# Kernel tuning notes

Hardware: AMD Instinct MI355X
Metric: run time of the kernel (lower is better)

Reference implementation:

```python
import jax, jax.numpy as jnp
import numpy as np


def setup_inputs() -> dict:
    key = jax.random.key(0)
    ks = jax.random.split(key, 5)
    B, Lq, Lk, KD, E, VD = 2, 1024, 1024, 128, 128, 128
    return {
        "query": jax.random.normal(ks[0], (B, Lq, KD), dtype=jnp.float32),
        "key": jax.random.normal(ks[1], (B, Lk, KD), dtype=jnp.float32),
        "value": jax.random.normal(ks[2], (B, Lk, VD), dtype=jnp.float32),
        "vT": jax.random.normal(ks[3], (E,), dtype=jnp.float32) * (1.0 / np.sqrt(E)),
        "weight": jax.random.normal(ks[4], (E, 2 * KD), dtype=jnp.float32) * (1.0 / np.sqrt(2 * KD)),
    }


def reference(query, key, value, vT, weight):
    # Additive (Bahdanau) attention: score(i,j) = vT . tanh(W @ concat(q_i, k_j))
    kdim = query.shape[-1]
    Wq = weight[:, :kdim]   # [E, kdim] acts on query half of concat
    Wk = weight[:, kdim:]   # [E, kdim] acts on key half
    qp = jnp.einsum("bqd,ed->bqe", query, Wq)   # [B, Lq, E]
    kp = jnp.einsum("bkd,ed->bke", key, Wk)     # [B, Lk, E]
    # broadcast-add replaces the explicit concat+linear: [B, Lq, Lk, E]
    h = jnp.tanh(qp[:, :, None, :] + kp[:, None, :, :])
    scores = jnp.einsum("bqke,e->bqk", h, vT)    # [B, Lq, Lk]
    attn = jax.nn.softmax(scores, axis=-1)
    return jnp.einsum("bqk,bkv->bqv", attn, value)  # [B, Lq, Vd]
```

## Files before the change

kernel.cpp:

```cpp
#include <hip/hip_runtime.h>

#define CSC 2.88539008177792681f

typedef float v2f __attribute__((ext_vector_type(2)));

__device__ __forceinline__ float fast_exp2(float x) {
  return __builtin_amdgcn_exp2f(x);
}
__device__ __forceinline__ float fast_rcp(float x) {
  return __builtin_amdgcn_rcpf(x);
}
__device__ __forceinline__ v2f vfma(v2f a, v2f b, v2f c) {
  return __builtin_elementwise_fma(a, b, c);
}
__device__ __forceinline__ v2f vsplat(float s) {
  v2f r;
  r[0] = s;
  r[1] = s;
  return r;
}

__global__ __launch_bounds__(256) void proj_kernel(
    const float* __restrict__ query, const float* __restrict__ key,
    const float* __restrict__ weight, float* __restrict__ Eq,
    float* __restrict__ EkT4) {
  __shared__ __align__(16) float rows[16][128];
  __shared__ __align__(16) float tile[16][132];
  int blk = blockIdx.x;
  bool isK = blk >= 128;
  const float* src = isK ? key : query;
  int woff = isK ? 128 : 0;
  int row0 = (isK ? blk - 128 : blk) * 16;
  int tid = threadIdx.x;
#pragma unroll
  for (int i = 0; i < 8; ++i) {
    int f = i * 256 + tid;
    rows[f >> 7][f & 127] = src[(size_t)row0 * 128 + f];
  }
  __syncthreads();
  int e = tid & 127;
  int rh = (tid >> 7) * 8;
  float acc[8];
#pragma unroll
  for (int i = 0; i < 8; ++i) acc[i] = 0.f;
  const float4* wrow =
      reinterpret_cast<const float4*>(weight + (size_t)e * 256 + woff);
#pragma unroll 4
  for (int d4 = 0; d4 < 32; ++d4) {
    float4 wv = wrow[d4];
#pragma unroll
    for (int i = 0; i < 8; ++i) {
      float4 rv = *reinterpret_cast<const float4*>(&rows[rh + i][d4 * 4]);
      acc[i] = fmaf(rv.x, wv.x, acc[i]);
      acc[i] = fmaf(rv.y, wv.y, acc[i]);
      acc[i] = fmaf(rv.z, wv.z, acc[i]);
      acc[i] = fmaf(rv.w, wv.w, acc[i]);
    }
  }
  if (!isK) {
#pragma unroll
    for (int i = 0; i < 8; ++i)
      Eq[(size_t)(row0 + rh + i) * 128 + e] = fast_exp2(CSC * acc[i]);
  } else {
#pragma unroll
    for (int i = 0; i < 8; ++i) tile[rh + i][e] = fast_exp2(CSC * acc[i]);
    __syncthreads();
    int kk = tid & 15;
    int e4a = tid >> 4;
#pragma unroll
    for (int h = 0; h < 2; ++h) {
      int ee = e4a + h * 16;
      float4 v = *reinterpret_cast<const float4*>(&tile[kk][ee * 4]);
      *reinterpret_cast<float4*>(EkT4 + ((size_t)ee * 2048 + row0 + kk) * 4) =
          v;
    }
  }
}

__global__ __launch_bounds__(512, 4) void attn_kernel(
    const float* __restrict__ Eq, const float* __restrict__ EkT4,
    const float* __restrict__ vT, const float* __restrict__ value,
    float* __restrict__ pblk, float* __restrict__ dsum) {
  __shared__ __align__(16) float sc[8][512];
  __shared__ __align__(16) v2f pout[8][8][64];
  __shared__ float wsum[8][8];

  int tid = threadIdx.x;
  int lane = tid & 63;
  int w = tid >> 6;
  int bi = blockIdx.x;
  int kh = bi & 1;
  int qg = (bi >> 1) & 127;
  int b = bi >> 8;
  int q0 = qg * 8;
  int k0 = kh * 512;

  {
    const float4* ekp = reinterpret_cast<const float4*>(EkT4) +
                        (size_t)b * 1024 + k0 + tid;
    const float* eqb = Eq + (size_t)(b * 1024 + q0) * 128;
    const float4* vtp = reinterpret_cast<const float4*>(vT);
    float acc[8];
#pragma unroll
    for (int q = 0; q < 8; ++q) acc[q] = 0.f;
#pragma unroll 2
    for (int e4 = 0; e4 < 32; ++e4) {
      float4 ek = ekp[(size_t)e4 * 2048];
      float4 vt4 = vtp[e4];
#pragma unroll
      for (int q = 0; q < 8; ++q) {
        float4 eqq = *reinterpret_cast<const float4*>(
            eqb + (size_t)q * 128 + e4 * 4);
        float A0 = fmaf(eqq.x, ek.x, 1.f);
        float A1 = fmaf(eqq.y, ek.y, 1.f);
        float A2 = fmaf(eqq.z, ek.z, 1.f);
        float A3 = fmaf(eqq.w, ek.w, 1.f);
        float P01 = A0 * A1;
        float P23 = A2 * A3;
        float t01 = fmaf(vt4.x, A1, vt4.y * A0);
        float t23 = fmaf(vt4.z, A3, vt4.w * A2);
        float num = fmaf(t23, P01, t01 * P23);
        acc[q] = fmaf(num, fast_rcp(P01 * P23), acc[q]);
      }
    }
#pragma unroll
    for (int q = 0; q < 8; ++q) {
      float p = fast_exp2(-CSC * acc[q]);
      sc[q][tid] = p;
      float s = p;
#pragma unroll
      for (int off = 32; off; off >>= 1) s += __shfl_xor(s, off);
      if (lane == 0) wsum[w][q] = s;
    }
  }
  __syncthreads();
  if (tid < 8) {
    float s = 0.f;
#pragma unroll
    for (int ww = 0; ww < 8; ++ww) s += wsum[ww][tid];
    dsum[(size_t)bi * 8 + tid] = s;
  }

  {
    int kb = w * 64;
    v2f acc2[8];
#pragma unroll
    for (int q = 0; q < 8; ++q) acc2[q] = vsplat(0.f);
    const v2f* vp = reinterpret_cast<const v2f*>(value) +
                    ((size_t)b * 1024 + k0 + kb) * 64 + lane;
#pragma unroll 2
    for (int k4 = 0; k4 < 16; ++k4) {
      v2f vv0 = vp[(size_t)(k4 * 4 + 0) * 64];
      v2f vv1 = vp[(size_t)(k4 * 4 + 1) * 64];
      v2f vv2 = vp[(size_t)(k4 * 4 + 2) * 64];
      v2f vv3 = vp[(size_t)(k4 * 4 + 3) * 64];
#pragma unroll
      for (int q = 0; q < 8; ++q) {
        float4 pp = *reinterpret_cast<const float4*>(&sc[q][kb + k4 * 4]);
        acc2[q] = vfma(vsplat(pp.x), vv0, acc2[q]);
        acc2[q] = vfma(vsplat(pp.y), vv1, acc2[q]);
        acc2[q] = vfma(vsplat(pp.z), vv2, acc2[q]);
        acc2[q] = vfma(vsplat(pp.w), vv3, acc2[q]);
      }
    }
#pragma unroll
    for (int q = 0; q < 8; ++q) pout[w][q][lane] = acc2[q];
  }
  __syncthreads();

  {
    int q = tid >> 6;
    int c = tid & 63;
    v2f r = pout[0][q][c];
#pragma unroll
    for (int ww = 1; ww < 8; ++ww) r = r + pout[ww][q][c];
    *reinterpret_cast<v2f*>(pblk + (size_t)bi * 1024 + q * 128 + 2 * c) = r;
  }
}

__global__ __launch_bounds__(512) void combine_kernel(
    const float* __restrict__ pblk, const float* __restrict__ dsum,
    float* __restrict__ out) {
  int g = blockIdx.x * 512 + threadIdx.x;
  int row = g >> 6;
  int c = g & 63;
  int b = row >> 10;
  int qg = (row >> 3) & 127;
  int q = row & 7;
  int bi0 = b * 256 + qg * 2;
  v2f r0 = *reinterpret_cast<const v2f*>(pblk + (size_t)bi0 * 1024 + q * 128 +
                                         2 * c);
  v2f r1 = *reinterpret_cast<const v2f*>(pblk + (size_t)(bi0 + 1) * 1024 +
                                         q * 128 + 2 * c);
  float d = dsum[(size_t)bi0 * 8 + q] + dsum[(size_t)(bi0 + 1) * 8 + q];
  v2f r = r0 + r1;
  float inv = fast_rcp(d);
  r[0] *= inv;
  r[1] *= inv;
  *reinterpret_cast<v2f*>(out + (size_t)row * 128 + 2 * c) = r;
}

extern "C" void kernel_launch(void* const* d_in, const int* in_sizes, int n_in,
                              void* d_out, int out_size, void* d_ws,
                              size_t ws_size, hipStream_t stream) {
  const float* query = (const float*)d_in[0];
  const float* key = (const float*)d_in[1];
  const float* value = (const float*)d_in[2];
  const float* vT = (const float*)d_in[3];
  const float* weight = (const float*)d_in[4];
  float* out = (float*)d_out;
  float* Eq = (float*)d_ws;
  float* EkT4 = Eq + 262144;
  float* pblk = EkT4 + 262144;
  float* dsum = pblk + 524288;
  proj_kernel<<<256, 256, 0, stream>>>(query, key, weight, Eq, EkT4);
  attn_kernel<<<512, 512, 0, stream>>>(Eq, EkT4, vT, value, pblk, dsum);
  combine_kernel<<<256, 512, 0, stream>>>(pblk, dsum, out);
}
```

Baseline: 48.55 us.

## Split attention keys into four chunks and stage Eq/vT in LDS

The attention kernel now splits each query group's keys into four 256-key chunks, handled by 256-thread blocks, instead of two 512-key chunks, doubling the grid to 1024 blocks. The per-block query exponentials and vT are loaded once into shared memory rather than re-read from global memory inside the inner loop. The combine kernel now sums four partial outputs and denominators, and the workspace layout grows to hold the larger partial buffer. This adds more blocks and more parallel work across CUs at the cost of extra partial-result traffic and a heavier combine step.

```diff
diff --git a/kernel.cpp b/kernel.cpp
--- a/kernel.cpp
+++ b/kernel.cpp
@@ -77,40 +77,51 @@
   }
 }
 
-__global__ __launch_bounds__(512, 4) void attn_kernel(
+__global__ __launch_bounds__(256, 4) void attn_kernel(
     const float* __restrict__ Eq, const float* __restrict__ EkT4,
     const float* __restrict__ vT, const float* __restrict__ value,
     float* __restrict__ pblk, float* __restrict__ dsum) {
-  __shared__ __align__(16) float sc[8][512];
-  __shared__ __align__(16) v2f pout[8][8][64];
-  __shared__ float wsum[8][8];
+  __shared__ __align__(16) float eq_lds[8][128];
+  __shared__ __align__(16) float vt_lds[128];
+  __shared__ __align__(16) float sc[8][256];
+  __shared__ __align__(16) v2f pout[4][8][64];
+  __shared__ float wsum[4][8];
 
   int tid = threadIdx.x;
   int lane = tid & 63;
   int w = tid >> 6;
   int bi = blockIdx.x;
-  int kh = bi & 1;
-  int qg = (bi >> 1) & 127;
-  int b = bi >> 8;
+  int kh = bi & 3;
+  int qg = (bi >> 2) & 127;
+  int b = bi >> 9;
   int q0 = qg * 8;
-  int k0 = kh * 512;
+  int k0 = kh * 256;
 
   {
-    const float4* ekp = reinterpret_cast<const float4*>(EkT4) +
-                        (size_t)b * 1024 + k0 + tid;
-    const float* eqb = Eq + (size_t)(b * 1024 + q0) * 128;
-    const float4* vtp = reinterpret_cast<const float4*>(vT);
+    const float4* eqg =
+        reinterpret_cast<const float4*>(Eq + (size_t)(b * 1024 + q0) * 128);
+    *reinterpret_cast<float4*>(&eq_lds[tid >> 5][(tid & 31) * 4]) = eqg[tid];
+    if (tid < 32)
+      *reinterpret_cast<float4*>(&vt_lds[tid * 4]) =
+          reinterpret_cast<const float4*>(vT)[tid];
+  }
+  __syncthreads();
+
+  {
+    const float4* ekp =
+        reinterpret_cast<const float4*>(EkT4) + (size_t)b * 1024 + k0 + tid;
     float acc[8];
 #pragma unroll
     for (int q = 0; q < 8; ++q) acc[q] = 0.f;
 #pragma unroll 2
     for (int e4 = 0; e4 < 32; ++e4) {
       float4 ek = ekp[(size_t)e4 * 2048];
-      float4 vt4 = vtp[e4];
+      float4 vt4 =
+          *reinterpret_cast<const float4*>(&vt_lds[e4 * 4]);
 #pragma unroll
       for (int q = 0; q < 8; ++q) {
-        float4 eqq = *reinterpret_cast<const float4*>(
-            eqb + (size_t)q * 128 + e4 * 4);
+        float4 eqq =
+            *reinterpret_cast<const float4*>(&eq_lds[q][e4 * 4]);
         float A0 = fmaf(eqq.x, ek.x, 1.f);
         float A1 = fmaf(eqq.y, ek.y, 1.f);
         float A2 = fmaf(eqq.z, ek.z, 1.f);
@@ -135,9 +146,7 @@
   }
   __syncthreads();
   if (tid < 8) {
-    float s = 0.f;
-#pragma unroll
-    for (int ww = 0; ww < 8; ++ww) s += wsum[ww][tid];
+    float s = wsum[0][tid] + wsum[1][tid] + wsum[2][tid] + wsum[3][tid];
     dsum[(size_t)bi * 8 + tid] = s;
   }
 
@@ -168,12 +177,12 @@
   }
   __syncthreads();
 
-  {
-    int q = tid >> 6;
-    int c = tid & 63;
+  for (int s = tid; s < 512; s += 256) {
+    int q = s >> 6;
+    int c = s & 63;
     v2f r = pout[0][q][c];
 #pragma unroll
-    for (int ww = 1; ww < 8; ++ww) r = r + pout[ww][q][c];
+    for (int ww = 1; ww < 4; ++ww) r = r + pout[ww][q][c];
     *reinterpret_cast<v2f*>(pblk + (size_t)bi * 1024 + q * 128 + 2 * c) = r;
   }
 }
@@ -187,13 +196,15 @@
   int b = row >> 10;
   int qg = (row >> 3) & 127;
   int q = row & 7;
-  int bi0 = b * 256 + qg * 2;
-  v2f r0 = *reinterpret_cast<const v2f*>(pblk + (size_t)bi0 * 1024 + q * 128 +
-                                         2 * c);
-  v2f r1 = *reinterpret_cast<const v2f*>(pblk + (size_t)(bi0 + 1) * 1024 +
-                                         q * 128 + 2 * c);
-  float d = dsum[(size_t)bi0 * 8 + q] + dsum[(size_t)(bi0 + 1) * 8 + q];
-  v2f r = r0 + r1;
+  int bi0 = b * 512 + qg * 4;
+  v2f r = vsplat(0.f);
+  float d = 0.f;
+#pragma unroll
+  for (int kh = 0; kh < 4; ++kh) {
+    r = r + *reinterpret_cast<const v2f*>(pblk + (size_t)(bi0 + kh) * 1024 +
+                                          q * 128 + 2 * c);
+    d += dsum[(size_t)(bi0 + kh) * 8 + q];
+  }
   float inv = fast_rcp(d);
   r[0] *= inv;
   r[1] *= inv;
@@ -212,8 +223,8 @@
   float* Eq = (float*)d_ws;
   float* EkT4 = Eq + 262144;
   float* pblk = EkT4 + 262144;
-  float* dsum = pblk + 524288;
+  float* dsum = pblk + 1048576;
   proj_kernel<<<256, 256, 0, stream>>>(query, key, weight, Eq, EkT4);
-  attn_kernel<<<512, 512, 0, stream>>>(Eq, EkT4, vT, value, pblk, dsum);
+  attn_kernel<<<1024, 256, 0, stream>>>(Eq, EkT4, vT, value, pblk, dsum);
   combine_kernel<<<256, 512, 0, stream>>>(pblk, dsum, out);
 }
```

Measured after the change: 54.51 us. 12.3% more time.

## Pack two keys per lane with packed-FP32 math and smaller query tiles

Applied to the files above, without the earlier changes.

Reorganizes the key-projection layout so each float4 holds two adjacent keys for two embedding dims, letting each thread handle two keys with v2f packed FMAs in the score loop. The attention block shrinks to 256 threads and 4 queries per block (1024 blocks), with each wave covering 128 keys in the value accumulation. The combine kernel and workspace indexing are adjusted to match. This aims to use packed FP32 throughput and raise block count, at the cost of less Eq reuse per EkT load and more blocks.

```diff
diff --git a/kernel.cpp b/kernel.cpp
--- a/kernel.cpp
+++ b/kernel.cpp
@@ -19,11 +19,23 @@
   r[1] = s;
   return r;
 }
+__device__ __forceinline__ v2f f4lo(const float4& a) {
+  v2f r;
+  r[0] = a.x;
+  r[1] = a.y;
+  return r;
+}
+__device__ __forceinline__ v2f f4hi(const float4& a) {
+  v2f r;
+  r[0] = a.z;
+  r[1] = a.w;
+  return r;
+}
 
 __global__ __launch_bounds__(256) void proj_kernel(
     const float* __restrict__ query, const float* __restrict__ key,
     const float* __restrict__ weight, float* __restrict__ Eq,
-    float* __restrict__ EkT4) {
+    float* __restrict__ EkT2) {
   __shared__ __align__(16) float rows[16][128];
   __shared__ __align__(16) float tile[16][132];
   int blk = blockIdx.x;
@@ -65,97 +77,111 @@
 #pragma unroll
     for (int i = 0; i < 8; ++i) tile[rh + i][e] = fast_exp2(CSC * acc[i]);
     __syncthreads();
-    int kk = tid & 15;
-    int e4a = tid >> 4;
+    int kpl = tid & 7;
+    int e2b = tid >> 3;
 #pragma unroll
     for (int h = 0; h < 2; ++h) {
-      int ee = e4a + h * 16;
-      float4 v = *reinterpret_cast<const float4*>(&tile[kk][ee * 4]);
-      *reinterpret_cast<float4*>(EkT4 + ((size_t)ee * 2048 + row0 + kk) * 4) =
-          v;
-    }
-  }
-}
-
-__global__ __launch_bounds__(512, 4) void attn_kernel(
-    const float* __restrict__ Eq, const float* __restrict__ EkT4,
+      int e2 = e2b + h * 32;
+      float4 v = make_float4(tile[2 * kpl][2 * e2], tile[2 * kpl + 1][2 * e2],
+                             tile[2 * kpl][2 * e2 + 1],
+                             tile[2 * kpl + 1][2 * e2 + 1]);
+      *reinterpret_cast<float4*>(
+          EkT2 + ((size_t)e2 * 1024 + (row0 >> 1) + kpl) * 4) = v;
+    }
+  }
+}
+
+__device__ __forceinline__ void quad4pk(const float4 eq, const float4 vt,
+                                        v2f ek0, v2f ek1, v2f ek2, v2f ek3,
+                                        v2f& acc) {
+  v2f one = vsplat(1.f);
+  v2f A0 = vfma(vsplat(eq.x), ek0, one);
+  v2f A1 = vfma(vsplat(eq.y), ek1, one);
+  v2f A2 = vfma(vsplat(eq.z), ek2, one);
+  v2f A3 = vfma(vsplat(eq.w), ek3, one);
+  v2f P01 = A0 * A1;
+  v2f P23 = A2 * A3;
+  v2f t01 = vfma(vsplat(vt.x), A1, vsplat(vt.y) * A0);
+  v2f t23 = vfma(vsplat(vt.z), A3, vsplat(vt.w) * A2);
+  v2f num = vfma(t23, P01, t01 * P23);
+  v2f den = P01 * P23;
+  v2f r;
+  r[0] = fast_rcp(den[0]);
+  r[1] = fast_rcp(den[1]);
+  acc = vfma(num, r, acc);
+}
+
+__global__ __launch_bounds__(256, 4) void attn_kernel(
+    const float* __restrict__ Eq, const float* __restrict__ EkT2,
     const float* __restrict__ vT, const float* __restrict__ value,
     float* __restrict__ pblk, float* __restrict__ dsum) {
-  __shared__ __align__(16) float sc[8][512];
-  __shared__ __align__(16) v2f pout[8][8][64];
-  __shared__ float wsum[8][8];
+  __shared__ __align__(16) float sc[4][512];
+  __shared__ __align__(16) v2f pout[4][4][64];
+  __shared__ float wsum[4][4];
 
   int tid = threadIdx.x;
   int lane = tid & 63;
   int w = tid >> 6;
   int bi = blockIdx.x;
   int kh = bi & 1;
-  int qg = (bi >> 1) & 127;
-  int b = bi >> 8;
-  int q0 = qg * 8;
+  int qg = (bi >> 1) & 255;
+  int b = bi >> 9;
+  int q0 = qg * 4;
   int k0 = kh * 512;
 
   {
-    const float4* ekp = reinterpret_cast<const float4*>(EkT4) +
-                        (size_t)b * 1024 + k0 + tid;
+    const float4* ekp = reinterpret_cast<const float4*>(EkT2) +
+                        (size_t)b * 512 + (k0 >> 1) + tid;
     const float* eqb = Eq + (size_t)(b * 1024 + q0) * 128;
     const float4* vtp = reinterpret_cast<const float4*>(vT);
-    float acc[8];
-#pragma unroll
-    for (int q = 0; q < 8; ++q) acc[q] = 0.f;
+    v2f acc[4];
+#pragma unroll
+    for (int q = 0; q < 4; ++q) acc[q] = vsplat(0.f);
 #pragma unroll 2
     for (int e4 = 0; e4 < 32; ++e4) {
-      float4 ek = ekp[(size_t)e4 * 2048];
+      float4 f4a = ekp[(size_t)(2 * e4 + 0) * 1024];
+      float4 f4b = ekp[(size_t)(2 * e4 + 1) * 1024];
+      v2f ek0 = f4lo(f4a), ek1 = f4hi(f4a), ek2 = f4lo(f4b), ek3 = f4hi(f4b);
       float4 vt4 = vtp[e4];
 #pragma unroll
-      for (int q = 0; q < 8; ++q) {
+      for (int q = 0; q < 4; ++q) {
         float4 eqq = *reinterpret_cast<const float4*>(
             eqb + (size_t)q * 128 + e4 * 4);
-        float A0 = fmaf(eqq.x, ek.x, 1.f);
-        float A1 = fmaf(eqq.y, ek.y, 1.f);
-        float A2 = fmaf(eqq.z, ek.z, 1.f);
-        float A3 = fmaf(eqq.w, ek.w, 1.f);
-        float P01 = A0 * A1;
-        float P23 = A2 * A3;
-        float t01 = fmaf(vt4.x, A1, vt4.y * A0);
-        float t23 = fmaf(vt4.z, A3, vt4.w * A2);
-        float num = fmaf(t23, P01, t01 * P23);
-        acc[q] = fmaf(num, fast_rcp(P01 * P23), acc[q]);
+        quad4pk(eqq, vt4, ek0, ek1, ek2, ek3, acc[q]);
       }
     }
 #pragma unroll
-    for (int q = 0; q < 8; ++q) {
-      float p = fast_exp2(-CSC * acc[q]);
-      sc[q][tid] = p;
-      float s = p;
+    for (int q = 0; q < 4; ++q) {
+      v2f p;
+      p[0] = fast_exp2(-CSC * acc[q][0]);
+      p[1] = fast_exp2(-CSC * acc[q][1]);
+      *reinterpret_cast<v2f*>(&sc[q][2 * tid]) = p;
+      float s = p[0] + p[1];
 #pragma unroll
       for (int off = 32; off; off >>= 1) s += __shfl_xor(s, off);
       if (lane == 0) wsum[w][q] = s;
     }
   }
   __syncthreads();
-  if (tid < 8) {
-    float s = 0.f;
-#pragma unroll
-    for (int ww = 0; ww < 8; ++ww) s += wsum[ww][tid];
-    dsum[(size_t)bi * 8 + tid] = s;
-  }
+  if (tid < 4)
+    dsum[(size_t)bi * 4 + tid] =
+        wsum[0][tid] + wsum[1][tid] + wsum[2][tid] + wsum[3][tid];
 
   {
-    int kb = w * 64;
-    v2f acc2[8];
-#pragma unroll
-    for (int q = 0; q < 8; ++q) acc2[q] = vsplat(0.f);
+    int kb = w * 128;
+    v2f acc2[4];
+#pragma unroll
+    for (int q = 0; q < 4; ++q) acc2[q] = vsplat(0.f);
     const v2f* vp = reinterpret_cast<const v2f*>(value) +
                     ((size_t)b * 1024 + k0 + kb) * 64 + lane;
 #pragma unroll 2
-    for (int k4 = 0; k4 < 16; ++k4) {
+    for (int k4 = 0; k4 < 32; ++k4) {
       v2f vv0 = vp[(size_t)(k4 * 4 + 0) * 64];
       v2f vv1 = vp[(size_t)(k4 * 4 + 1) * 64];
       v2f vv2 = vp[(size_t)(k4 * 4 + 2) * 64];
       v2f vv3 = vp[(size_t)(k4 * 4 + 3) * 64];
 #pragma unroll
-      for (int q = 0; q < 8; ++q) {
+      for (int q = 0; q < 4; ++q) {
         float4 pp = *reinterpret_cast<const float4*>(&sc[q][kb + k4 * 4]);
         acc2[q] = vfma(vsplat(pp.x), vv0, acc2[q]);
         acc2[q] = vfma(vsplat(pp.y), vv1, acc2[q]);
@@ -164,7 +190,7 @@
       }
     }
 #pragma unroll
-    for (int q = 0; q < 8; ++q) pout[w][q][lane] = acc2[q];
+    for (int q = 0; q < 4; ++q) pout[w][q][lane] = acc2[q];
   }
   __syncthreads();
 
@@ -173,26 +199,24 @@
     int c = tid & 63;
     v2f r = pout[0][q][c];
 #pragma unroll
-    for (int ww = 1; ww < 8; ++ww) r = r + pout[ww][q][c];
-    *reinterpret_cast<v2f*>(pblk + (size_t)bi * 1024 + q * 128 + 2 * c) = r;
-  }
-}
-
-__global__ __launch_bounds__(512) void combine_kernel(
+    for (int ww = 1; ww < 4; ++ww) r = r + pout[ww][q][c];
+    *reinterpret_cast<v2f*>(pblk + (size_t)bi * 512 + q * 128 + 2 * c) = r;
+  }
+}
+
+__global__ __launch_bounds__(256) void combine_kernel(
     const float* __restrict__ pblk, const float* __restrict__ dsum,
     float* __restrict__ out) {
-  int g = blockIdx.x * 512 + threadIdx.x;
+  int g = blockIdx.x * 256 + threadIdx.x;
   int row = g >> 6;
   int c = g & 63;
-  int b = row >> 10;
-  int qg = (row >> 3) & 127;
-  int q = row & 7;
-  int bi0 = b * 256 + qg * 2;
-  v2f r0 = *reinterpret_cast<const v2f*>(pblk + (size_t)bi0 * 1024 + q * 128 +
+  int q = row & 3;
+  int bi0 = (row >> 2) * 2;
+  v2f r0 = *reinterpret_cast<const v2f*>(pblk + (size_t)bi0 * 512 + q * 128 +
                                          2 * c);
-  v2f r1 = *reinterpret_cast<const v2f*>(pblk + (size_t)(bi0 + 1) * 1024 +
+  v2f r1 = *reinterpret_cast<const v2f*>(pblk + (size_t)(bi0 + 1) * 512 +
                                          q * 128 + 2 * c);
-  float d = dsum[(size_t)bi0 * 8 + q] + dsum[(size_t)(bi0 + 1) * 8 + q];
+  float d = dsum[(size_t)bi0 * 4 + q] + dsum[(size_t)(bi0 + 1) * 4 + q];
   v2f r = r0 + r1;
   float inv = fast_rcp(d);
   r[0] *= inv;
@@ -210,10 +234,10 @@
   const float* weight = (const float*)d_in[4];
   float* out = (float*)d_out;
   float* Eq = (float*)d_ws;
-  float* EkT4 = Eq + 262144;
-  float* pblk = EkT4 + 262144;
+  float* EkT2 = Eq + 262144;
+  float* pblk = EkT2 + 262144;
   float* dsum = pblk + 524288;
-  proj_kernel<<<256, 256, 0, stream>>>(query, key, weight, Eq, EkT4);
-  attn_kernel<<<512, 512, 0, stream>>>(Eq, EkT4, vT, value, pblk, dsum);
-  combine_kernel<<<256, 512, 0, stream>>>(pblk, dsum, out);
-}
+  proj_kernel<<<256, 256, 0, stream>>>(query, key, weight, Eq, EkT2);
+  attn_kernel<<<1024, 256, 0, stream>>>(Eq, EkT2, vT, value, pblk, dsum);
+  combine_kernel<<<512, 256, 0, stream>>>(pblk, dsum, out);
+}
```

After: 50.53 us. 4.1% more time.
